# Kernel optimization log

Hardware: AMD Instinct MI355X
Metric: run time of the kernel (lower is better)

Reference implementation:

```python
import jax, jax.numpy as jnp
import numpy as np

NV0 = 30000
NE0 = 90000          # edges at level 0 -> 2*NE0 half-flaps
D = 32               # Dout: per-vertex feature dim (first 3 channels = xyz)
DHID = 128
NUM_SUBD = 2
NV1 = NV0 + NE0      # vertices after one subdivision (even + odd)
NE1 = 3 * NE0        # edges at level 1
DIN_MLP = 4 * D - 3  # flattened half-flap feature minus leading (0,0,0)


def _make_hfidx(key, nV, nHF):
    # 4 distinct vertex indices per half-flap; column 0 covers every vertex
    k0, k1, k2, k3 = jax.random.split(key, 4)
    c0 = jnp.concatenate([jnp.arange(nV), jax.random.randint(k0, (nHF - nV,), 0, nV)])
    o1 = jax.random.randint(k1, (nHF,), 1, nV // 3)
    o2 = jax.random.randint(k2, (nHF,), nV // 3, 2 * nV // 3)
    o3 = jax.random.randint(k3, (nHF,), 2 * nV // 3, nV - 1)
    return jnp.stack([c0, (c0 + o1) % nV, (c0 + o2) % nV, (c0 + o3) % nV], axis=1)


def setup_inputs():
    key = jax.random.key(0)
    ks = jax.random.split(key, 6)
    fv = jax.random.normal(ks[0], (NV0, D), dtype=jnp.float32)
    hfIdx0 = _make_hfidx(ks[1], NV0, 2 * NE0)
    hfIdx1 = _make_hfidx(ks[2], NV1, 2 * NE1)
    s = 0.05
    W_in = jax.random.normal(ks[3], (2 * NUM_SUBD, DIN_MLP, DHID), dtype=jnp.float32) * s
    b_in = jnp.zeros((2 * NUM_SUBD, DHID), dtype=jnp.float32)
    W_h = jax.random.normal(ks[4], (2 * NUM_SUBD, DHID, DHID), dtype=jnp.float32) * s
    b_h = jnp.zeros((2 * NUM_SUBD, DHID), dtype=jnp.float32)
    W_out = jax.random.normal(ks[5], (2 * NUM_SUBD, DHID, D), dtype=jnp.float32) * s
    b_out = jnp.zeros((2 * NUM_SUBD, D), dtype=jnp.float32)
    return {"fv": fv, "W_in": W_in, "b_in": b_in, "W_h": W_h, "b_h": b_h,
            "W_out": W_out, "b_out": b_out, "hfIdx0": hfIdx0, "hfIdx1": hfIdx1}


def _unit(v):
    return v / jnp.linalg.norm(v, axis=-1, keepdims=True)


def _flap_normalize(hf):
    # hf: [H, 4, D]; first 3 channels are world positions -> local frame coords
    V = hf[:, :, :3]
    v0, v1, v2, v3 = V[:, 0], V[:, 1], V[:, 2], V[:, 3]
    b1 = _unit(v1 - v0)
    fn0 = _unit(jnp.cross(v1 - v0, v2 - v0))   # face (0,1,2) normal
    fn1 = _unit(jnp.cross(v0 - v1, v3 - v1))   # face (1,0,3) normal
    b3 = _unit(fn0 + fn1)                       # edge normal
    b2 = jnp.cross(b3, b1)
    LF = jnp.stack([b1, b2, b3], axis=1)        # [H,3,3] local frames
    pos = jnp.einsum('hij,hkj->hik', V - v0[:, None, :], LF)  # bmm(pos, LF^T)
    hf_n = jnp.concatenate([pos, hf[:, :, 3:]], axis=-1)
    hf_n = hf_n.reshape(hf_n.shape[0], -1)[:, 3:]  # drop leading (0,0,0)
    return hf_n, LF


def _mlp(x, Wi, bi, Wh, bh, Wo, bo):
    x = jax.nn.relu(x @ Wi + bi)
    x = jax.nn.relu(x @ Wh + bh)
    return x @ Wo + bo


def _local2global(h, LF):
    pos = jnp.einsum('hi,hij->hj', h[:, :3], LF)  # c0*b1 + c1*b2 + c2*b3
    return jnp.concatenate([pos, h[:, 3:]], axis=1)


def _one_ring_pool(fhf, seg, nV):
    dof = jax.ops.segment_sum(jnp.ones((seg.shape[0],), fhf.dtype), seg, num_segments=nV)
    return jax.ops.segment_sum(fhf, seg, num_segments=nV) / dof[:, None]


def _half_edge_pool(fhe):
    # AvgPool2d((2,1)) over [2*nE, C] -> [nE, C]
    H, C = fhe.shape
    return fhe.reshape(H // 2, 2, C).mean(axis=1)


def _level(fv, hfIdx, pv, pe):
    nV = fv.shape[0]
    seg = hfIdx[:, 0]
    prev_pos = fv[:, :3]
    # even-vertex update: gather flaps -> local frames -> MLP -> unrotate -> pool
    fhf, LF = _flap_normalize(fv[hfIdx])
    fhf = _local2global(_mlp(fhf, *pv), LF)
    fv = _one_ring_pool(fhf, seg, nV)
    fv = jnp.concatenate([fv[:, :3] + prev_pos, fv[:, 3:]], axis=1)
    # odd-vertex (edge midpoint) update
    Ve = _half_edge_pool((fv[hfIdx[:, 0], :3] + fv[hfIdx[:, 1], :3]) * 0.5)
    fhf, LF = _flap_normalize(fv[hfIdx])
    fv_odd = _half_edge_pool(_local2global(_mlp(fhf, *pe), LF))
    fv_odd = jnp.concatenate([fv_odd[:, :3] + Ve, fv_odd[:, 3:]], axis=1)
    return jnp.concatenate([fv, fv_odd], axis=0)


def reference(fv, W_in, b_in, W_h, b_h, W_out, b_out, hfIdx0, hfIdx1):
    hfs = (hfIdx0, hfIdx1)
    outputs = [fv[:, :3]]
    for ii in range(NUM_SUBD):
        pv = (W_in[2 * ii], b_in[2 * ii], W_h[2 * ii], b_h[2 * ii], W_out[2 * ii], b_out[2 * ii])
        pe = (W_in[2 * ii + 1], b_in[2 * ii + 1], W_h[2 * ii + 1], b_h[2 * ii + 1], W_out[2 * ii + 1], b_out[2 * ii + 1])
        fv = _level(fv, hfs[ii], pv, pe)
        outputs.append(fv[:, :3])
    return tuple(outputs)
```

## Files before the change

### kernel.cpp

```cpp
#include <hip/hip_runtime.h>

#define NV0 30000
#define NE0 90000
#define H0 (2*NE0)
#define NV1 (NV0+NE0)
#define NE1 (3*NE0)
#define H1 (2*NE1)
#define DF 32
#define DH 128

typedef unsigned short bf16_t;
typedef unsigned int u32;
typedef __attribute__((ext_vector_type(8))) short short8;
typedef __attribute__((ext_vector_type(4))) float f32x4;

__device__ __forceinline__ float bf2f(bf16_t b) { return __uint_as_float(((u32)b) << 16); }
__device__ __forceinline__ bf16_t f2bf(float f) {
  u32 u = __float_as_uint(f);
  return (bf16_t)((u + 0x7fffu + ((u >> 16) & 1u)) >> 16);
}
__device__ __forceinline__ u32 pack2bf(float a, float b) {
  return (u32)f2bf(a) | ((u32)f2bf(b) << 16);
}
__device__ __forceinline__ float load_f(const void* p, long i, int isf32) {
  return isf32 ? ((const float*)p)[i] : bf2f(((const bf16_t*)p)[i]);
}
__device__ __forceinline__ void store_out(void* p, long i, float v, int isf32) {
  if (isf32) ((float*)p)[i] = v;
  else ((bf16_t*)p)[i] = f2bf(v);
}

__device__ __forceinline__ void lds_fence() {
  asm volatile("" ::: "memory");
  __builtin_amdgcn_sched_barrier(0);
}

struct F3 { float x, y, z; };
__device__ __forceinline__ F3 mkf3(float x, float y, float z){ F3 r; r.x=x; r.y=y; r.z=z; return r; }
__device__ __forceinline__ F3 f3sub(F3 a, F3 b){ return mkf3(a.x-b.x, a.y-b.y, a.z-b.z); }
__device__ __forceinline__ F3 f3add(F3 a, F3 b){ return mkf3(a.x+b.x, a.y+b.y, a.z+b.z); }
__device__ __forceinline__ float f3dot(F3 a, F3 b){ return a.x*b.x + a.y*b.y + a.z*b.z; }
__device__ __forceinline__ F3 f3crs(F3 a, F3 b){
  return mkf3(a.y*b.z - a.z*b.y, a.z*b.x - a.x*b.z, a.x*b.y - a.y*b.x);
}
__device__ __forceinline__ F3 f3nrm(F3 a){
  float r = rsqrtf(f3dot(a,a));
  return mkf3(a.x*r, a.y*r, a.z*r);
}

__global__ __launch_bounds__(256) void detect_kernel(const u32* __restrict__ fvw,
                                                     int* __restrict__ flag) {
  __shared__ int cnt;
  if (threadIdx.x == 0) cnt = 0;
  __syncthreads();
  int c = 0;
  #pragma unroll
  for (int j = 0; j < 2; ++j) {
    u32 w = fvw[threadIdx.x * 2 + j];
    u32 e = (w >> 7) & 0xffu;
    if (e > 140u) c++;
  }
  if (c) atomicAdd(&cnt, c);
  __syncthreads();
  if (threadIdx.x == 0) *flag = (cnt > 8) ? 1 : 0;
}

__global__ __launch_bounds__(256) void cvt_weights_kernel(const void* __restrict__ src,
                                                          float* __restrict__ dst, int n,
                                                          const int* __restrict__ flag) {
  int t = blockIdx.x * 256 + threadIdx.x;
  if (t >= n) return;
  dst[t] = load_f(src, t, *flag);
}

__global__ __launch_bounds__(256) void pt_win_kernel(const void* __restrict__ W_in,
                                                     bf16_t* __restrict__ dst,
                                                     const int* __restrict__ flag) {
  int t = blockIdx.x * 256 + threadIdx.x;
  if (t >= 4 * DH * DH) return;
  int s = t >> 14, n = (t >> 7) & 127, k = t & 127;
  float v = (k >= 3) ? load_f(W_in, (long)s * (125 * DH) + (k - 3) * DH + n, *flag) : 0.f;
  dst[t] = f2bf(v);
}
__global__ __launch_bounds__(256) void pt_wh_kernel(const void* __restrict__ W_h,
                                                    bf16_t* __restrict__ dst,
                                                    const int* __restrict__ flag) {
  int t = blockIdx.x * 256 + threadIdx.x;
  if (t >= 4 * DH * DH) return;
  int s = t >> 14, n = (t >> 7) & 127, k = t & 127;
  dst[t] = f2bf(load_f(W_h, (long)s * (DH * DH) + k * DH + n, *flag));
}
__global__ __launch_bounds__(256) void pt_wo_kernel(const void* __restrict__ W_out,
                                                    bf16_t* __restrict__ dst,
                                                    const int* __restrict__ flag) {
  int t = blockIdx.x * 256 + threadIdx.x;
  if (t >= 4 * 32 * DH) return;
  int s = t >> 12, n = (t >> 7) & 31, k = t & 127;
  dst[t] = f2bf(load_f(W_out, (long)s * (DH * 32) + k * 32 + n, *flag));
}

__global__ __launch_bounds__(256) void cvt_out0_kernel(const void* __restrict__ fv,
                                                       void* __restrict__ out,
                                                       const int* __restrict__ flag) {
  int t = blockIdx.x * 256 + threadIdx.x;
  if (t >= NV0 * 3) return;
  int v = t / 3, c = t - v * 3;
  if (*flag) ((float*)out)[t] = ((const float*)fv)[v * DF + c];
  else ((bf16_t*)out)[t] = ((const bf16_t*)fv)[v * DF + c];
}

#define XST 136

__device__ __forceinline__ f32x4 mfma16(short8 a, short8 b, f32x4 c) {
  return __builtin_amdgcn_mfma_f32_16x16x32_bf16(a, b, c, 0, 0, 0);
}

__device__ __forceinline__ void mlp_layer2(
    short* buf,
    const bf16_t* __restrict__ Wt, const float* __restrict__ bias,
    int m0, int arow, int koff, int rrow)
{
  lds_fence();
  short8 af[2][4];
  #pragma unroll
  for (int mt = 0; mt < 2; ++mt)
    #pragma unroll
    for (int kq = 0; kq < 4; ++kq)
      af[mt][kq] = *(const short8*)(buf + (m0 + mt * 16 + arow) * XST + kq * 32 + koff);
  lds_fence();
  #pragma unroll
  for (int ntl = 0; ntl < 8; ntl += 2) {
    f32x4 a00 = {0.f,0.f,0.f,0.f}, a01 = {0.f,0.f,0.f,0.f};
    f32x4 a10 = {0.f,0.f,0.f,0.f}, a11 = {0.f,0.f,0.f,0.f};
    #pragma unroll
    for (int kq = 0; kq < 4; ++kq) {
      short8 w0 = *(const short8*)(Wt + (ntl * 16 + arow) * DH + kq * 32 + koff);
      short8 w1 = *(const short8*)(Wt + ((ntl + 1) * 16 + arow) * DH + kq * 32 + koff);
      a00 = mfma16(af[0][kq], w0, a00);
      a01 = mfma16(af[0][kq], w1, a01);
      a10 = mfma16(af[1][kq], w0, a10);
      a11 = mfma16(af[1][kq], w1, a11);
    }
    int c0 = ntl * 16 + arow, c1 = c0 + 16;
    float bb0 = bias[c0], bb1 = bias[c1];
    #pragma unroll
    for (int r = 0; r < 4; ++r) {
      int rmA = m0 + rrow + r, rmB = m0 + 16 + rrow + r;
      buf[rmA * XST + c0] = (short)f2bf(fmaxf(a00[r] + bb0, 0.f));
      buf[rmA * XST + c1] = (short)f2bf(fmaxf(a01[r] + bb1, 0.f));
      buf[rmB * XST + c0] = (short)f2bf(fmaxf(a10[r] + bb0, 0.f));
      buf[rmB * XST + c1] = (short)f2bf(fmaxf(a11[r] + bb1, 0.f));
    }
  }
  lds_fence();
}

template<int MODE, int RAW>
__global__ __launch_bounds__(256, 4) void mlp3_kernel(
    const void* __restrict__ fvin, const int* __restrict__ hfIdx, int nH,
    const bf16_t* __restrict__ Wt1, const bf16_t* __restrict__ Wt2,
    const bf16_t* __restrict__ Wt3,
    const float* __restrict__ b1, const float* __restrict__ b2,
    const float* __restrict__ b3,
    float* __restrict__ outp, float* __restrict__ dofp,
    const int* __restrict__ flag)
{
  __shared__ __align__(16) short Xl[128 * XST];
  __shared__ float LFl[128 * 9];
  __shared__ int   idxl[128];

  const int t = threadIdx.x;
  const int lane = t & 63;
  const int m0 = (t >> 6) * 32;
  const int arow = lane & 15;
  const int koff = (lane >> 4) * 8;
  const int rrow = (lane >> 4) * 4;
  const int isf32 = RAW ? *flag : 1;

  const int nwg = gridDim.x;
  const int q = nwg >> 3, r = nwg & 7;
  const int xcd = blockIdx.x & 7;
  const int loc = blockIdx.x >> 3;
  const int bswz = (xcd < r ? xcd * (q + 1) : r * (q + 1) + (xcd - r) * q) + loc;
  const long h0 = (long)bswz * 128;

  #pragma unroll
  for (int half = 0; half < 2; ++half) {
    const int m = m0 + half * 16 + (lane >> 2);
    const int v = lane & 3;
    const long h = h0 + m;
    int vid = (h < nH) ? hfIdx[h * 4 + v] : 0;
    if (v == 0) idxl[m] = vid;
    float px, py, pz;
    u32 w[16];
    if (RAW && !isf32) {
      const uint4* src = (const uint4*)((const bf16_t*)fvin + (size_t)vid * DF);
      #pragma unroll
      for (int j = 0; j < 4; ++j) {
        uint4 x = src[j];
        w[j * 4 + 0] = x.x; w[j * 4 + 1] = x.y;
        w[j * 4 + 2] = x.z; w[j * 4 + 3] = x.w;
      }
      px = bf2f((bf16_t)(w[0] & 0xffff));
      py = bf2f((bf16_t)(w[0] >> 16));
      pz = bf2f((bf16_t)(w[1] & 0xffff));
    } else {
      const float4* src = (const float4*)((const float*)fvin + (size_t)vid * DF);
      float4 x0 = src[0];
      px = x0.x; py = x0.y; pz = x0.z;
      w[0] = pack2bf(x0.x, x0.y); w[1] = pack2bf(x0.z, x0.w);
      #pragma unroll
      for (int j = 1; j < 8; ++j) {
        float4 x = src[j];
        w[j * 2 + 0] = pack2bf(x.x, x.y);
        w[j * 2 + 1] = pack2bf(x.z, x.w);
      }
    }
    const int bl = lane & ~3;
    F3 p0 = mkf3(__shfl(px, bl),     __shfl(py, bl),     __shfl(pz, bl));
    F3 p1 = mkf3(__shfl(px, bl | 1), __shfl(py, bl | 1), __shfl(pz, bl | 1));
    F3 p2 = mkf3(__shfl(px, bl | 2), __shfl(py, bl | 2), __shfl(pz, bl | 2));
    F3 p3 = mkf3(__shfl(px, bl | 3), __shfl(py, bl | 3), __shfl(pz, bl | 3));
    F3 e1  = f3sub(p1, p0);
    F3 B1  = f3nrm(e1);
    F3 fn0 = f3nrm(f3crs(e1, f3sub(p2, p0)));
    F3 fn1 = f3nrm(f3crs(f3sub(p0, p1), f3sub(p3, p1)));
    F3 B3  = f3nrm(f3add(fn0, fn1));
    F3 B2  = f3crs(B3, B1);
    if (v == 0) {
      float* lf = LFl + m * 9;
      lf[0] = B1.x; lf[1] = B1.y; lf[2] = B1.z;
      lf[3] = B2.x; lf[4] = B2.y; lf[5] = B2.z;
      lf[6] = B3.x; lf[7] = B3.y; lf[8] = B3.z;
    } else {
      F3 d = f3sub(mkf3(px, py, pz), p0);
      w[0] = pack2bf(f3dot(d, B1), f3dot(d, B2));
      w[1] = (w[1] & 0xffff0000u) | (u32)f2bf(f3dot(d, B3));
    }
    uint4* xrow = (uint4*)(Xl + m * XST + v * 32);
    #pragma unroll
    for (int j = 0; j < 4; ++j)
      xrow[j] = make_uint4(w[j * 4 + 0], w[j * 4 + 1], w[j * 4 + 2], w[j * 4 + 3]);
  }

  mlp_layer2(Xl, Wt1, b1, m0, arow, koff, rrow);
  mlp_layer2(Xl, Wt2, b2, m0, arow, koff, rrow);

  {
    lds_fence();
    short8 af[2][4];
    #pragma unroll
    for (int mt = 0; mt < 2; ++mt)
      #pragma unroll
      for (int kq = 0; kq < 4; ++kq)
        af[mt][kq] = *(const short8*)(Xl + (m0 + mt * 16 + arow) * XST + kq * 32 + koff);
    f32x4 a00 = {0.f,0.f,0.f,0.f}, a01 = {0.f,0.f,0.f,0.f};
    f32x4 a10 = {0.f,0.f,0.f,0.f}, a11 = {0.f,0.f,0.f,0.f};
    #pragma unroll
    for (int kq = 0; kq < 4; ++kq) {
      short8 w0 = *(const short8*)(Wt3 + arow * DH + kq * 32 + koff);
      short8 w1 = *(const short8*)(Wt3 + (16 + arow) * DH + kq * 32 + koff);
      a00 = mfma16(af[0][kq], w0, a00);
      a01 = mfma16(af[0][kq], w1, a01);
      a10 = mfma16(af[1][kq], w0, a10);
      a11 = mfma16(af[1][kq], w1, a11);
    }
    lds_fence();
    float* Yf = (float*)Xl;
    float bb0 = b3[arow], bb1 = b3[16 + arow];
    #pragma unroll
    for (int r = 0; r < 4; ++r) {
      int rmA = m0 + rrow + r, rmB = m0 + 16 + rrow + r;
      Yf[rmA * 68 + arow]      = a00[r] + bb0;
      Yf[rmA * 68 + 16 + arow] = a01[r] + bb1;
      Yf[rmB * 68 + arow]      = a10[r] + bb0;
      Yf[rmB * 68 + 16 + arow] = a11[r] + bb1;
    }
  }
  lds_fence();

  float* Yf = (float*)Xl;
  #pragma unroll
  for (int i = 0; i < 16; ++i) {
    int row = m0 + i * 2 + (lane >> 5);
    long h = h0 + row;
    int ch = lane & 31;
    float val = 0.f;
    if (h < nH) {
      val = Yf[row * 68 + ch];
      if (ch < 3) {
        float y0 = Yf[row * 68 + 0], y1 = Yf[row * 68 + 1], y2 = Yf[row * 68 + 2];
        val = y0 * LFl[row * 9 + ch] + y1 * LFl[row * 9 + 3 + ch] + y2 * LFl[row * 9 + 6 + ch];
      }
    }
    if (MODE == 0) {
      if (h < nH) {
        atomicAdd(&outp[(size_t)idxl[row] * DF + ch], val);
        if (ch == 0) atomicAdd(&dofp[idxl[row]], 1.f);
      }
    } else {
      float sum = val + __shfl_xor(val, 32);
      if (h < nH && lane < 32) {
        if (MODE == 1) outp[(size_t)(h >> 1) * DF + ch] = 0.5f * sum;
        else if (ch < 3) outp[(size_t)(h >> 1) * 3 + ch] = 0.5f * sum;
      }
    }
  }
}

template<int RAW>
__global__ __launch_bounds__(256) void finalize_even_kernel(
    float* buf, const float* __restrict__ dof,
    const void* __restrict__ prevraw, const float* __restrict__ prevf,
    void* __restrict__ out, int outbase, const int* __restrict__ flag, int nV) {
  int t = blockIdx.x * 256 + threadIdx.x;
  if (t >= nV * DF) return;
  int v = t >> 5, c = t & 31;
  float val = buf[t] / fmaxf(dof[v], 1.0f);
  if (c < 3) {
    float pp = RAW ? load_f(prevraw, (long)v * DF + c, *flag) : prevf[(long)v * DF + c];
    val += pp;
    store_out(out, (long)outbase + (long)v * 3 + c, val, *flag);
  }
  buf[t] = val;
}

__global__ __launch_bounds__(256) void finalize_odd_full_kernel(
    float* oddbuf, const int* __restrict__ hfIdx,
    const float* fveven, void* __restrict__ out, int outbase,
    const int* __restrict__ flag, int nE, int nVeven) {
  int t = blockIdx.x * 256 + threadIdx.x;
  if (t >= nE * DF) return;
  int e = t >> 5, c = t & 31;
  float val = oddbuf[t];
  if (c < 3) {
    int a0 = hfIdx[(size_t)(2 * e) * 4 + 0];
    int a1 = hfIdx[(size_t)(2 * e) * 4 + 1];
    int b0 = hfIdx[(size_t)(2 * e + 1) * 4 + 0];
    int b1 = hfIdx[(size_t)(2 * e + 1) * 4 + 1];
    val += 0.25f * (fveven[(size_t)a0 * DF + c] + fveven[(size_t)a1 * DF + c] +
                    fveven[(size_t)b0 * DF + c] + fveven[(size_t)b1 * DF + c]);
    store_out(out, (long)outbase + (long)(nVeven + e) * 3 + c, val, *flag);
  }
  oddbuf[t] = val;
}

__global__ __launch_bounds__(256) void finalize_odd_pos_kernel(
    const float* __restrict__ odd3, const int* __restrict__ hfIdx,
    const float* __restrict__ fveven, void* __restrict__ out, int outbase,
    const int* __restrict__ flag, int nE, int nVeven) {
  int t = blockIdx.x * 256 + threadIdx.x;
  if (t >= nE * 3) return;
  int e = t / 3, c = t - e * 3;
  int a0 = hfIdx[(size_t)(2 * e) * 4 + 0];
  int a1 = hfIdx[(size_t)(2 * e) * 4 + 1];
  int b0 = hfIdx[(size_t)(2 * e + 1) * 4 + 0];
  int b1 = hfIdx[(size_t)(2 * e + 1) * 4 + 1];
  float val = odd3[t] + 0.25f * (fveven[(size_t)a0 * DF + c] + fveven[(size_t)a1 * DF + c] +
                                 fveven[(size_t)b0 * DF + c] + fveven[(size_t)b1 * DF + c]);
  store_out(out, (long)outbase + (long)(nVeven + e) * 3 + c, val, *flag);
}

extern "C" void kernel_launch(void* const* d_in, const int* in_sizes, int n_in,
                              void* d_out, int out_size, void* d_ws, size_t ws_size,
                              hipStream_t stream) {
  const void* fv    = d_in[0];
  const void* W_in  = d_in[1];
  const void* b_in  = d_in[2];
  const void* W_h   = d_in[3];
  const void* b_h   = d_in[4];
  const void* W_out = d_in[5];
  const void* b_out = d_in[6];
  const int* hf0 = (const int*)d_in[7];
  const int* hf1 = (const int*)d_in[8];
  (void)in_sizes; (void)n_in; (void)out_size;

  float* fv1   = (float*)d_ws;
  float* fvup2 = fv1   + 3840000;
  float* dof   = fvup2 + 3840000;
  float* bif   = dof   + 120000;
  float* bhf   = bif   + 512;
  float* bof   = bhf   + 512;
  int*   flag  = (int*)(bof + 128);
  bf16_t* Wti  = (bf16_t*)(flag + 4);
  bf16_t* Wth  = Wti + 65536;
  bf16_t* Wto  = Wth + 65536;
  const size_t needed = ((size_t)3840000 * 2 + 120000 + 512 * 2 + 128 + 4) * 4
                      + (65536 * 2 + 16384) * 2;
  if (ws_size < needed) return;

  float* odd_acc0 = fv1 + (size_t)NV0 * DF;

  detect_kernel<<<1, 256, 0, stream>>>((const u32*)fv, flag);
  pt_win_kernel<<<256, 256, 0, stream>>>(W_in, Wti, flag);
  pt_wh_kernel<<<256, 256, 0, stream>>>(W_h, Wth, flag);
  pt_wo_kernel<<<64, 256, 0, stream>>>(W_out, Wto, flag);
  cvt_weights_kernel<<<2, 256, 0, stream>>>(b_in, bif, 512, flag);
  cvt_weights_kernel<<<2, 256, 0, stream>>>(b_h, bhf, 512, flag);
  cvt_weights_kernel<<<1, 256, 0, stream>>>(b_out, bof, 128, flag);
  cvt_out0_kernel<<<(NV0 * 3 + 255) / 256, 256, 0, stream>>>(fv, d_out, flag);

  const int G0 = (H0 + 127) / 128, G1 = (H1 + 127) / 128;

  hipMemsetAsync(fv1, 0, (size_t)NV0 * DF * 4, stream);
  hipMemsetAsync(dof, 0, (size_t)NV0 * 4, stream);
  mlp3_kernel<0, 1><<<G0, 256, 0, stream>>>(fv, hf0, H0,
      Wti + 0 * 16384, Wth + 0 * 16384, Wto + 0 * 4096,
      bif + 0 * DH, bhf + 0 * DH, bof + 0 * DF, fv1, dof, flag);
  finalize_even_kernel<1><<<(NV0 * DF + 255) / 256, 256, 0, stream>>>(
      fv1, dof, fv, nullptr, d_out, 90000, flag, NV0);
  mlp3_kernel<1, 0><<<G0, 256, 0, stream>>>(fv1, hf0, H0,
      Wti + 1 * 16384, Wth + 1 * 16384, Wto + 1 * 4096,
      bif + 1 * DH, bhf + 1 * DH, bof + 1 * DF, odd_acc0, nullptr, flag);
  finalize_odd_full_kernel<<<(NE0 * DF + 255) / 256, 256, 0, stream>>>(
      odd_acc0, hf0, fv1, d_out, 90000, flag, NE0, NV0);

  hipMemsetAsync(fvup2, 0, (size_t)NV1 * DF * 4, stream);
  hipMemsetAsync(dof, 0, (size_t)NV1 * 4, stream);
  mlp3_kernel<0, 0><<<G1, 256, 0, stream>>>(fv1, hf1, H1,
      Wti + 2 * 16384, Wth + 2 * 16384, Wto + 2 * 4096,
      bif + 2 * DH, bhf + 2 * DH, bof + 2 * DF, fvup2, dof, flag);
  finalize_even_kernel<0><<<(NV1 * DF + 255) / 256, 256, 0, stream>>>(
      fvup2, dof, nullptr, fv1, d_out, 450000, flag, NV1);
  mlp3_kernel<2, 0><<<G1, 256, 0, stream>>>(fvup2, hf1, H1,
      Wti + 3 * 16384, Wth + 3 * 16384, Wto + 3 * 4096,
      bif + 3 * DH, bhf + 3 * DH, bof + 3 * DF, fv1, nullptr, flag);
  finalize_odd_pos_kernel<<<(NE1 * 3 + 255) / 256, 256, 0, stream>>>(
      fv1, hf1, fvup2, d_out, 450000, flag, NE1, NV1);
}
```

Measured before the change: 637.5 us.

## Prefetch next-layer weights, batch both half gathers, use DPP quad broadcasts

The first weight tile of each MLP layer is now loaded one stage ahead (during the gather and during the previous layer) and passed through in registers. The two half-row vertex gathers are issued together before any frame computation, giving more loads in flight. Quad broadcasts of vertex positions use DPP moves instead of __shfl. The cost is higher register pressure under launch_bounds(256,4), which could cause spills or lower occupancy.

```diff
diff --git a/kernel.cpp b/kernel.cpp
--- a/kernel.cpp
+++ b/kernel.cpp
@@ -35,6 +35,11 @@
   __builtin_amdgcn_sched_barrier(0);
 }
 
+__device__ __forceinline__ float qb0(float x){ return __int_as_float(__builtin_amdgcn_mov_dpp(__float_as_int(x), 0x00, 0xf, 0xf, true)); }
+__device__ __forceinline__ float qb1(float x){ return __int_as_float(__builtin_amdgcn_mov_dpp(__float_as_int(x), 0x55, 0xf, 0xf, true)); }
+__device__ __forceinline__ float qb2(float x){ return __int_as_float(__builtin_amdgcn_mov_dpp(__float_as_int(x), 0xAA, 0xf, 0xf, true)); }
+__device__ __forceinline__ float qb3(float x){ return __int_as_float(__builtin_amdgcn_mov_dpp(__float_as_int(x), 0xFF, 0xf, 0xf, true)); }
+
 struct F3 { float x, y, z; };
 __device__ __forceinline__ F3 mkf3(float x, float y, float z){ F3 r; r.x=x; r.y=y; r.z=z; return r; }
 __device__ __forceinline__ F3 f3sub(F3 a, F3 b){ return mkf3(a.x-b.x, a.y-b.y, a.z-b.z); }
@@ -115,9 +120,19 @@
   return __builtin_amdgcn_mfma_f32_16x16x32_bf16(a, b, c, 0, 0, 0);
 }
 
-__device__ __forceinline__ void mlp_layer2(
+typedef struct { short8 w[4]; } W4;
+__device__ __forceinline__ W4 loadW4(const bf16_t* __restrict__ Wt, int arow, int koff) {
+  W4 r;
+  #pragma unroll
+  for (int kq = 0; kq < 4; ++kq)
+    r.w[kq] = *(const short8*)(Wt + arow * DH + kq * 32 + koff);
+  return r;
+}
+
+__device__ __forceinline__ W4 mlp_layer2(
     short* buf,
     const bf16_t* __restrict__ Wt, const float* __restrict__ bias,
+    W4 wpre, const bf16_t* __restrict__ Wtnext,
     int m0, int arow, int koff, int rrow)
 {
   lds_fence();
@@ -127,6 +142,7 @@
     #pragma unroll
     for (int kq = 0; kq < 4; ++kq)
       af[mt][kq] = *(const short8*)(buf + (m0 + mt * 16 + arow) * XST + kq * 32 + koff);
+  W4 wnext = loadW4(Wtnext, arow, koff);
   lds_fence();
   #pragma unroll
   for (int ntl = 0; ntl < 8; ntl += 2) {
@@ -134,7 +150,8 @@
     f32x4 a10 = {0.f,0.f,0.f,0.f}, a11 = {0.f,0.f,0.f,0.f};
     #pragma unroll
     for (int kq = 0; kq < 4; ++kq) {
-      short8 w0 = *(const short8*)(Wt + (ntl * 16 + arow) * DH + kq * 32 + koff);
+      short8 w0 = (ntl == 0) ? wpre.w[kq]
+                 : *(const short8*)(Wt + (ntl * 16 + arow) * DH + kq * 32 + koff);
       short8 w1 = *(const short8*)(Wt + ((ntl + 1) * 16 + arow) * DH + kq * 32 + koff);
       a00 = mfma16(af[0][kq], w0, a00);
       a01 = mfma16(af[0][kq], w1, a01);
@@ -153,6 +170,55 @@
     }
   }
   lds_fence();
+  return wnext;
+}
+
+template<int ISF32>
+__device__ __forceinline__ void frame_store(const float4* xf, const uint4* xr,
+                                            int m, int v, short* Xl, float* LFl) {
+  u32 w[16];
+  float px, py, pz;
+  if (ISF32) {
+    px = xf[0].x; py = xf[0].y; pz = xf[0].z;
+    #pragma unroll
+    for (int j = 0; j < 8; ++j) {
+      w[2 * j]     = pack2bf(xf[j].x, xf[j].y);
+      w[2 * j + 1] = pack2bf(xf[j].z, xf[j].w);
+    }
+  } else {
+    #pragma unroll
+    for (int j = 0; j < 4; ++j) {
+      w[4 * j + 0] = xr[j].x; w[4 * j + 1] = xr[j].y;
+      w[4 * j + 2] = xr[j].z; w[4 * j + 3] = xr[j].w;
+    }
+    px = bf2f((bf16_t)(w[0] & 0xffff));
+    py = bf2f((bf16_t)(w[0] >> 16));
+    pz = bf2f((bf16_t)(w[1] & 0xffff));
+  }
+  F3 p0 = mkf3(qb0(px), qb0(py), qb0(pz));
+  F3 p1 = mkf3(qb1(px), qb1(py), qb1(pz));
+  F3 p2 = mkf3(qb2(px), qb2(py), qb2(pz));
+  F3 p3 = mkf3(qb3(px), qb3(py), qb3(pz));
+  F3 e1  = f3sub(p1, p0);
+  F3 B1  = f3nrm(e1);
+  F3 fn0 = f3nrm(f3crs(e1, f3sub(p2, p0)));
+  F3 fn1 = f3nrm(f3crs(f3sub(p0, p1), f3sub(p3, p1)));
+  F3 B3  = f3nrm(f3add(fn0, fn1));
+  F3 B2  = f3crs(B3, B1);
+  if (v == 0) {
+    float* lf = LFl + m * 9;
+    lf[0] = B1.x; lf[1] = B1.y; lf[2] = B1.z;
+    lf[3] = B2.x; lf[4] = B2.y; lf[5] = B2.z;
+    lf[6] = B3.x; lf[7] = B3.y; lf[8] = B3.z;
+  } else {
+    F3 d = f3sub(mkf3(px, py, pz), p0);
+    w[0] = pack2bf(f3dot(d, B1), f3dot(d, B2));
+    w[1] = (w[1] & 0xffff0000u) | (u32)f2bf(f3dot(d, B3));
+  }
+  uint4* xrow = (uint4*)(Xl + m * XST + v * 32);
+  #pragma unroll
+  for (int j = 0; j < 4; ++j)
+    xrow[j] = make_uint4(w[4 * j], w[4 * j + 1], w[4 * j + 2], w[4 * j + 3]);
 }
 
 template<int MODE, int RAW>
@@ -184,67 +250,40 @@
   const int bswz = (xcd < r ? xcd * (q + 1) : r * (q + 1) + (xcd - r) * q) + loc;
   const long h0 = (long)bswz * 128;
 
-  #pragma unroll
-  for (int half = 0; half < 2; ++half) {
-    const int m = m0 + half * 16 + (lane >> 2);
+  W4 wp = loadW4(Wt1, arow, koff);
+
+  {
+    const int mA = m0 + (lane >> 2), mB = mA + 16;
     const int v = lane & 3;
-    const long h = h0 + m;
-    int vid = (h < nH) ? hfIdx[h * 4 + v] : 0;
-    if (v == 0) idxl[m] = vid;
-    float px, py, pz;
-    u32 w[16];
+    const long hA = h0 + mA, hB = h0 + mB;
+    int vidA = (hA < nH) ? hfIdx[hA * 4 + v] : 0;
+    int vidB = (hB < nH) ? hfIdx[hB * 4 + v] : 0;
+    if (v == 0) { idxl[mA] = vidA; idxl[mB] = vidB; }
     if (RAW && !isf32) {
-      const uint4* src = (const uint4*)((const bf16_t*)fvin + (size_t)vid * DF);
+      uint4 rA[4], rB[4];
+      const uint4* sA = (const uint4*)((const bf16_t*)fvin + (size_t)vidA * DF);
+      const uint4* sB = (const uint4*)((const bf16_t*)fvin + (size_t)vidB * DF);
       #pragma unroll
-      for (int j = 0; j < 4; ++j) {
-        uint4 x = src[j];
-        w[j * 4 + 0] = x.x; w[j * 4 + 1] = x.y;
-        w[j * 4 + 2] = x.z; w[j * 4 + 3] = x.w;
-      }
-      px = bf2f((bf16_t)(w[0] & 0xffff));
-      py = bf2f((bf16_t)(w[0] >> 16));
-      pz = bf2f((bf16_t)(w[1] & 0xffff));
+      for (int j = 0; j < 4; ++j) rA[j] = sA[j];
+      #pragma unroll
+      for (int j = 0; j < 4; ++j) rB[j] = sB[j];
+      frame_store<0>(nullptr, rA, mA, v, Xl, LFl);
+      frame_store<0>(nullptr, rB, mB, v, Xl, LFl);
     } else {
-      const float4* src = (const float4*)((const float*)fvin + (size_t)vid * DF);
-      float4 x0 = src[0];
-      px = x0.x; py = x0.y; pz = x0.z;
-      w[0] = pack2bf(x0.x, x0.y); w[1] = pack2bf(x0.z, x0.w);
+      float4 xA[8], xB[8];
+      const float4* sA = (const float4*)((const float*)fvin + (size_t)vidA * DF);
+      const float4* sB = (const float4*)((const float*)fvin + (size_t)vidB * DF);
       #pragma unroll
-      for (int j = 1; j < 8; ++j) {
-        float4 x = src[j];
-        w[j * 2 + 0] = pack2bf(x.x, x.y);
-        w[j * 2 + 1] = pack2bf(x.z, x.w);
-      }
-    }
-    const int bl = lane & ~3;
-    F3 p0 = mkf3(__shfl(px, bl),     __shfl(py, bl),     __shfl(pz, bl));
-    F3 p1 = mkf3(__shfl(px, bl | 1), __shfl(py, bl | 1), __shfl(pz, bl | 1));
-    F3 p2 = mkf3(__shfl(px, bl | 2), __shfl(py, bl | 2), __shfl(pz, bl | 2));
-    F3 p3 = mkf3(__shfl(px, bl | 3), __shfl(py, bl | 3), __shfl(pz, bl | 3));
-    F3 e1  = f3sub(p1, p0);
-    F3 B1  = f3nrm(e1);
-    F3 fn0 = f3nrm(f3crs(e1, f3sub(p2, p0)));
-    F3 fn1 = f3nrm(f3crs(f3sub(p0, p1), f3sub(p3, p1)));
-    F3 B3  = f3nrm(f3add(fn0, fn1));
-    F3 B2  = f3crs(B3, B1);
-    if (v == 0) {
-      float* lf = LFl + m * 9;
-      lf[0] = B1.x; lf[1] = B1.y; lf[2] = B1.z;
-      lf[3] = B2.x; lf[4] = B2.y; lf[5] = B2.z;
-      lf[6] = B3.x; lf[7] = B3.y; lf[8] = B3.z;
-    } else {
-      F3 d = f3sub(mkf3(px, py, pz), p0);
-      w[0] = pack2bf(f3dot(d, B1), f3dot(d, B2));
-      w[1] = (w[1] & 0xffff0000u) | (u32)f2bf(f3dot(d, B3));
-    }
-    uint4* xrow = (uint4*)(Xl + m * XST + v * 32);
-    #pragma unroll
-    for (int j = 0; j < 4; ++j)
-      xrow[j] = make_uint4(w[j * 4 + 0], w[j * 4 + 1], w[j * 4 + 2], w[j * 4 + 3]);
-  }
-
-  mlp_layer2(Xl, Wt1, b1, m0, arow, koff, rrow);
-  mlp_layer2(Xl, Wt2, b2, m0, arow, koff, rrow);
+      for (int j = 0; j < 8; ++j) xA[j] = sA[j];
+      #pragma unroll
+      for (int j = 0; j < 8; ++j) xB[j] = sB[j];
+      frame_store<1>(xA, nullptr, mA, v, Xl, LFl);
+      frame_store<1>(xB, nullptr, mB, v, Xl, LFl);
+    }
+  }
+
+  wp = mlp_layer2(Xl, Wt1, b1, wp, Wt2, m0, arow, koff, rrow);
+  wp = mlp_layer2(Xl, Wt2, b2, wp, Wt3, m0, arow, koff, rrow);
 
   {
     lds_fence();
@@ -258,7 +297,7 @@
     f32x4 a10 = {0.f,0.f,0.f,0.f}, a11 = {0.f,0.f,0.f,0.f};
     #pragma unroll
     for (int kq = 0; kq < 4; ++kq) {
-      short8 w0 = *(const short8*)(Wt3 + arow * DH + kq * 32 + koff);
+      short8 w0 = wp.w[kq];
       short8 w1 = *(const short8*)(Wt3 + (16 + arow) * DH + kq * 32 + koff);
       a00 = mfma16(af[0][kq], w0, a00);
       a01 = mfma16(af[0][kq], w1, a01);
```

Result: slower. 682.7 us (+7.1%).
